# Kernel optimization log

Measured on AMD Instinct MI355X. Metric: run time of the kernel, lower is better.

The kernel has to match this reference:

```python
import jax, jax.numpy as jnp
from jax import lax
import numpy as np

B, T, F = 2048, 256, 64
HIDDEN = [64, 32, 16]
OUT = 1


def _lstm_params(key, in_dim, h):
    k1, k2, k3 = jax.random.split(key, 3)
    s_in = 1.0 / np.sqrt(in_dim)
    s_h = 1.0 / np.sqrt(h)
    W = jax.random.uniform(k1, (in_dim, 4 * h), jnp.float32, -s_in, s_in)
    U = jax.random.uniform(k2, (h, 4 * h), jnp.float32, -s_h, s_h)
    # Keras unit_forget_bias: bias starts at 0 except forget gate = 1
    b = jnp.concatenate([jnp.zeros((h,)), jnp.ones((h,)), jnp.zeros((2 * h,))]).astype(jnp.float32)
    return W, U, b


def setup_inputs() -> dict:
    key = jax.random.key(0)
    ks = jax.random.split(key, 6)
    x = jax.random.normal(ks[0], (B, T, F), jnp.float32)
    W0, U0, b0 = _lstm_params(ks[1], F, HIDDEN[0])
    W1, U1, b1 = _lstm_params(ks[2], HIDDEN[0], HIDDEN[1])
    W2, U2, b2 = _lstm_params(ks[3], HIDDEN[1], HIDDEN[2])
    s = 1.0 / np.sqrt(HIDDEN[2])
    Wd = jax.random.uniform(ks[4], (HIDDEN[2], OUT), jnp.float32, -s, s)
    bd = jnp.zeros((OUT,), jnp.float32)
    return {"x": x, "W0": W0, "U0": U0, "b0": b0,
            "W1": W1, "U1": U1, "b1": b1,
            "W2": W2, "U2": U2, "b2": b2,
            "Wd": Wd, "bd": bd}


def _lstm(x, W, U, b):
    """Keras-style LSTM scan. x: [B,T,in]. Returns (seq [B,T,H], last_h [B,H]).
    Gate order i,f,g,o; recurrent_activation=sigmoid, activation=tanh.
    Dropout/recurrent_dropout are identity at inference (training=False)."""
    Bsz = x.shape[0]
    H = U.shape[0]
    # precompute input projection for all timesteps (one big GEMM)
    xz = jnp.einsum('bti,ig->btg', x, W) + b  # [B,T,4H]
    xz_t = jnp.swapaxes(xz, 0, 1)  # [T,B,4H]

    def step(carry, z_in):
        h, c = carry
        z = z_in + h @ U  # [B,4H]
        i, f, g, o = jnp.split(z, 4, axis=-1)
        i = jax.nn.sigmoid(i)
        f = jax.nn.sigmoid(f)
        g = jnp.tanh(g)
        o = jax.nn.sigmoid(o)
        c = f * c + i * g
        h = o * jnp.tanh(c)
        return (h, c), h

    init = (jnp.zeros((Bsz, H), x.dtype), jnp.zeros((Bsz, H), x.dtype))
    (h_last, _), hs = lax.scan(step, init, xz_t)
    return jnp.swapaxes(hs, 0, 1), h_last


def reference(x, W0, U0, b0, W1, U1, b1, W2, U2, b2, Wd, bd):
    h, _ = _lstm(x, W0, U0, b0)          # return_sequences=True -> [B,T,64]
    h, _ = _lstm(h, W1, U1, b1)          # return_sequences=True -> [B,T,32]
    _, h_last = _lstm(h, W2, U2, b2)     # return_sequences=False -> [B,16]
    return h_last @ Wd + bd              # Dense -> [B,1]
```

## Files before the change

kernel.cpp:

```cpp
#include <hip/hip_runtime.h>


typedef __attribute__((ext_vector_type(8))) short s8v;
typedef __attribute__((ext_vector_type(4))) float f4v;
typedef __attribute__((ext_vector_type(2))) unsigned uint2v;
typedef unsigned short ushort_t;

#define T_STEPS 256
#define BT 8

#define XH  0
#define XL  2048
#define H0H 4096
#define H0L 6144
#define H1H 8192
#define H1L 9216
#define H2H 10240
#define H2L 11264
#define SM_SHORTS 12288

#define PIN(v) asm volatile("" : "+v"(v))
#define BAR()  asm volatile("s_waitcnt lgkmcnt(0)\n\ts_barrier" ::: "memory")

__device__ __forceinline__ unsigned short f2bf(float f) {
    unsigned u = __float_as_uint(f);
    u += 0x7fff + ((u >> 16) & 1);
    return (unsigned short)(u >> 16);
}
__device__ __forceinline__ float bf2f(unsigned short s) {
    return __uint_as_float(((unsigned)s) << 16);
}
__device__ __forceinline__ void tsplit(float v, unsigned short& hi, unsigned short& lo) {
    unsigned u = __float_as_uint(v);
    hi = (unsigned short)(u >> 16);
    float r = v - __uint_as_float(u & 0xffff0000u);
    lo = (unsigned short)(__float_as_uint(r) >> 16);
}
__device__ __forceinline__ float sigmoid_f(float x) {
    return __builtin_amdgcn_rcpf(1.0f + __expf(-x));
}
__device__ __forceinline__ float tanh_f(float x) {
    return 1.0f - 2.0f * __builtin_amdgcn_rcpf(__expf(2.0f * x) + 1.0f);
}

__device__ __forceinline__ float sel_swap(float a, float b) {
    uint2v r = __builtin_amdgcn_permlane32_swap(__float_as_uint(a), __float_as_uint(b), false, false);
    return __uint_as_float(r[0]);
}

__device__ __forceinline__ float wval(const float* W, const float* U,
                                      int inDim, int KH, int fourH, int k, int n) {
    if (k < inDim) return W[k * fourH + n];
    if (k < KH)    return U[(k - inDim) * fourH + n];
    return 0.0f;
}
__device__ __forceinline__ void load_bfrag(const float* W, const float* U,
                                           int inDim, int KH, int fourH,
                                           int k0, int n, s8v& hi, s8v& lo) {
#pragma unroll
    for (int j = 0; j < 8; ++j) {
        float w = wval(W, U, inDim, KH, fourH, k0 + j, n);
        unsigned short h = f2bf(w);
        unsigned short l = f2bf(w - bf2f(h));
        hi[j] = (short)h;
        lo[j] = (short)l;
    }
}

__device__ __forceinline__ void gates2(const f4v* acc, float* c, float* hn) {
#pragma unroll
    for (int j = 0; j < 2; ++j) {
        float zi = sel_swap(acc[0][j], acc[0][j + 2]);
        float zf = sel_swap(acc[1][j], acc[1][j + 2]);
        float zg = sel_swap(acc[2][j], acc[2][j + 2]);
        float zo = sel_swap(acc[3][j], acc[3][j + 2]);
        float ig = sigmoid_f(zi);
        float fg = sigmoid_f(zf);
        float gg = tanh_f(zg);
        float og = sigmoid_f(zo);
        c[j] = fmaf(fg, c[j], ig * gg);
        hn[j] = og * tanh_f(c[j]);
    }
}

__global__ __attribute__((amdgpu_flat_work_group_size(512, 512),
                          amdgpu_waves_per_eu(2, 2)))
void lstm_pipe(const float* __restrict__ x,
               const float* __restrict__ W0, const float* __restrict__ U0, const float* __restrict__ b0,
               const float* __restrict__ W1, const float* __restrict__ U1, const float* __restrict__ b1,
               const float* __restrict__ W2, const float* __restrict__ U2, const float* __restrict__ b2,
               const float* __restrict__ Wd, const float* __restrict__ bd,
               float* __restrict__ out)
{
    const int tid  = threadIdx.x;
    const int lane = tid & 63;
    const int wv   = tid >> 6;
    const int fr   = lane >> 4;
    const int fc   = lane & 15;
    const int bbase = blockIdx.x * BT;

    __shared__ __align__(16) ushort_t SMEM[SM_SHORTS];
    __shared__ __align__(16) float h2last[BT][16];

    {
        unsigned* p32 = (unsigned*)SMEM;
        for (int i = tid; i < SM_SHORTS / 2; i += 512) p32[i] = 0u;
    }
    __syncthreads();

    const ushort_t* rb = SMEM + lane * 8;
    const int rowb = (fr & 1) * 4 + ((fr >> 1) << 1);

    if (wv < 4) {
        s8v Bh[4][4], Bl[4][4];
        float bias[4];
#pragma unroll
        for (int g = 0; g < 4; ++g) {
            int n = g * 64 + wv * 16 + fc;
            bias[g] = b0[n];
#pragma unroll
            for (int kc = 0; kc < 4; ++kc)
                load_bfrag(W0, U0, 64, 128, 256, kc * 32 + fr * 8, n, Bh[g][kc], Bl[g][kc]);
        }
#pragma unroll
        for (int g = 0; g < 4; ++g) {
            PIN(bias[g]);
#pragma unroll
            for (int kc = 0; kc < 4; ++kc) { PIN(Bh[g][kc]); PIN(Bl[g][kc]); }
        }
        float c0[2] = {0.f, 0.f};
        const int hq  = wv >> 1;
        const int k   = (wv & 1) * 16 + fc;
        const int ibw = (k >> 3) * 128 + (k & 7);
        __syncthreads();
        for (int s = 0; s < T_STEPS + 2; ++s) {
            if (s < T_STEPS) {
                const ushort_t* r = rb + ((s & 1) << 10);
                s8v ah[4], al[4];
                ah[0] = *(const s8v*)&r[XH  +   0];
                al[0] = *(const s8v*)&r[XL  +   0];
                ah[1] = *(const s8v*)&r[XH  + 512];
                al[1] = *(const s8v*)&r[XL  + 512];
                ah[2] = *(const s8v*)&r[H0H +   0];
                al[2] = *(const s8v*)&r[H0L +   0];
                ah[3] = *(const s8v*)&r[H0H + 512];
                al[3] = *(const s8v*)&r[H0L + 512];
                f4v acc[4];
#pragma unroll
                for (int g = 0; g < 4; ++g) acc[g] = (f4v){bias[g], bias[g], bias[g], bias[g]};
#pragma unroll
                for (int kc = 0; kc < 4; ++kc) {
#pragma unroll
                    for (int g = 0; g < 4; ++g)
                        acc[g] = __builtin_amdgcn_mfma_f32_16x16x32_bf16(ah[kc], Bh[g][kc], acc[g], 0, 0, 0);
#pragma unroll
                    for (int g = 0; g < 4; ++g)
                        acc[g] = __builtin_amdgcn_mfma_f32_16x16x32_bf16(al[kc], Bh[g][kc], acc[g], 0, 0, 0);
#pragma unroll
                    for (int g = 0; g < 4; ++g)
                        acc[g] = __builtin_amdgcn_mfma_f32_16x16x32_bf16(ah[kc], Bl[g][kc], acc[g], 0, 0, 0);
                }
                float hn[2];
                gates2(acc, c0, hn);
                {
                    ushort_t* w = SMEM + (((s & 1) ^ 1) << 10) + hq * 512 + ibw;
#pragma unroll
                    for (int j = 0; j < 2; ++j) {
                        unsigned short hh_, ll_;
                        tsplit(hn[j], hh_, ll_);
                        w[H0H + (rowb + j) * 8] = hh_;
                        w[H0L + (rowb + j) * 8] = ll_;
                    }
                }
            }
            BAR();
        }
    } else if (wv < 6) {
        s8v Bh[4][3], Bl[4][3];
        float bias[4];
#pragma unroll
        for (int g = 0; g < 4; ++g) {
            int n = g * 32 + (wv & 1) * 16 + fc;
            bias[g] = b1[n];
#pragma unroll
            for (int kc = 0; kc < 3; ++kc)
                load_bfrag(W1, U1, 64, 96, 128, kc * 32 + fr * 8, n, Bh[g][kc], Bl[g][kc]);
        }
#pragma unroll
        for (int g = 0; g < 4; ++g) {
            PIN(bias[g]);
#pragma unroll
            for (int kc = 0; kc < 3; ++kc) { PIN(Bh[g][kc]); PIN(Bl[g][kc]); }
        }
        float c1[2] = {0.f, 0.f};
        const int k   = (wv & 1) * 16 + fc;
        const int ibw = (k >> 3) * 128 + (k & 7);
        __syncthreads();
        for (int s = 0; s < T_STEPS + 2; ++s) {
            if (s >= 1 && s <= T_STEPS) {
                const int p = s & 1;
                const ushort_t* r  = rb + (p << 10);
                const ushort_t* r1 = rb + (p << 9);
                s8v ah[3], al[3];
                ah[0] = *(const s8v*)&r[H0H +   0];
                al[0] = *(const s8v*)&r[H0L +   0];
                ah[1] = *(const s8v*)&r[H0H + 512];
                al[1] = *(const s8v*)&r[H0L + 512];
                ah[2] = *(const s8v*)&r1[H1H];
                al[2] = *(const s8v*)&r1[H1L];
                f4v acc[4];
#pragma unroll
                for (int g = 0; g < 4; ++g) acc[g] = (f4v){bias[g], bias[g], bias[g], bias[g]};
#pragma unroll
                for (int kc = 0; kc < 3; ++kc) {
#pragma unroll
                    for (int g = 0; g < 4; ++g)
                        acc[g] = __builtin_amdgcn_mfma_f32_16x16x32_bf16(ah[kc], Bh[g][kc], acc[g], 0, 0, 0);
#pragma unroll
                    for (int g = 0; g < 4; ++g)
                        acc[g] = __builtin_amdgcn_mfma_f32_16x16x32_bf16(al[kc], Bh[g][kc], acc[g], 0, 0, 0);
#pragma unroll
                    for (int g = 0; g < 4; ++g)
                        acc[g] = __builtin_amdgcn_mfma_f32_16x16x32_bf16(ah[kc], Bl[g][kc], acc[g], 0, 0, 0);
                }
                float hn[2];
                gates2(acc, c1, hn);
                {
                    ushort_t* w = SMEM + ((p ^ 1) << 9) + ibw;
#pragma unroll
                    for (int j = 0; j < 2; ++j) {
                        unsigned short hh_, ll_;
                        tsplit(hn[j], hh_, ll_);
                        w[H1H + (rowb + j) * 8] = hh_;
                        w[H1L + (rowb + j) * 8] = ll_;
                    }
                }
            }
            BAR();
        }
    } else if (wv == 6) {
        s8v Bh[4][2], Bl[4][2];
        float bias[4];
#pragma unroll
        for (int g = 0; g < 4; ++g) {
            int n = g * 16 + fc;
            bias[g] = b2[n];
#pragma unroll
            for (int kc = 0; kc < 2; ++kc)
                load_bfrag(W2, U2, 32, 48, 64, kc * 32 + fr * 8, n, Bh[g][kc], Bl[g][kc]);
        }
#pragma unroll
        for (int g = 0; g < 4; ++g) {
            PIN(bias[g]);
#pragma unroll
            for (int kc = 0; kc < 2; ++kc) { PIN(Bh[g][kc]); PIN(Bl[g][kc]); }
        }
        float c2[2] = {0.f, 0.f};
        const int ibw = (fc >> 3) * 128 + (fc & 7);
        __syncthreads();
        for (int s = 0; s < T_STEPS + 2; ++s) {
            if (s >= 2) {
                const int p = s & 1;
                const ushort_t* r1 = rb + (p << 9);
                s8v ah[2], al[2];
                ah[0] = *(const s8v*)&r1[H1H];
                al[0] = *(const s8v*)&r1[H1L];
                ah[1] = *(const s8v*)&r1[H2H];
                al[1] = *(const s8v*)&r1[H2L];
                f4v acc[4];
#pragma unroll
                for (int g = 0; g < 4; ++g) acc[g] = (f4v){bias[g], bias[g], bias[g], bias[g]};
#pragma unroll
                for (int kc = 0; kc < 2; ++kc) {
#pragma unroll
                    for (int g = 0; g < 4; ++g)
                        acc[g] = __builtin_amdgcn_mfma_f32_16x16x32_bf16(ah[kc], Bh[g][kc], acc[g], 0, 0, 0);
#pragma unroll
                    for (int g = 0; g < 4; ++g)
                        acc[g] = __builtin_amdgcn_mfma_f32_16x16x32_bf16(al[kc], Bh[g][kc], acc[g], 0, 0, 0);
#pragma unroll
                    for (int g = 0; g < 4; ++g)
                        acc[g] = __builtin_amdgcn_mfma_f32_16x16x32_bf16(ah[kc], Bl[g][kc], acc[g], 0, 0, 0);
                }
                float hn[2];
                gates2(acc, c2, hn);
                {
                    ushort_t* w = SMEM + ((p ^ 1) << 9) + ibw;
#pragma unroll
                    for (int j = 0; j < 2; ++j) {
                        unsigned short hh_, ll_;
                        tsplit(hn[j], hh_, ll_);
                        w[H2H + (rowb + j) * 8] = hh_;
                        w[H2L + (rowb + j) * 8] = ll_;
                    }
                    if (s == T_STEPS + 1) {
#pragma unroll
                        for (int j = 0; j < 2; ++j) h2last[rowb + j][fc] = hn[j];
                    }
                }
            }
            BAR();
        }
    } else {
        const int xb = lane >> 3;
        const int fo = (lane & 7) * 8;
        const float* xp = x + ((size_t)(bbase + xb) * T_STEPS) * 64 + fo;
        const int o2 = (fo >> 5) * 512 + (((fo & 31) >> 3) * 16 + xb) * 8;

        auto write_x = [&](float4 v0, float4 v1, int tt) {
            float vv[8] = {v0.x, v0.y, v0.z, v0.w, v1.x, v1.y, v1.z, v1.w};
            s8v hi8, lo8;
#pragma unroll
            for (int j = 0; j < 8; ++j) {
                unsigned short h_, l_;
                tsplit(vv[j], h_, l_);
                hi8[j] = (short)h_;
                lo8[j] = (short)l_;
            }
            ushort_t* wbp = SMEM + ((tt & 1) << 10) + o2;
            *(s8v*)&wbp[XH] = hi8;
            *(s8v*)&wbp[XL] = lo8;
        };

        float4 pa = *(const float4*)(xp);
        float4 pb = *(const float4*)(xp + 4);
        write_x(pa, pb, 0);
        pa = *(const float4*)(xp + 64);
        pb = *(const float4*)(xp + 64 + 4);
        __syncthreads();
        for (int s = 0; s < T_STEPS + 2; ++s) {
            float4 na, nb;
            const bool ld = (s + 2 < T_STEPS);
            if (ld) {
                na = *(const float4*)(xp + (size_t)(s + 2) * 64);
                nb = *(const float4*)(xp + (size_t)(s + 2) * 64 + 4);
            }
            if (s + 1 < T_STEPS) write_x(pa, pb, s + 1);
            if (ld) { pa = na; pb = nb; }
            BAR();
        }
    }

    __syncthreads();
    if (tid < BT) {
        float acc = bd[0];
#pragma unroll
        for (int j = 0; j < 16; ++j) acc += h2last[tid][j] * Wd[j];
        out[bbase + tid] = acc;
    }
}

extern "C" void kernel_launch(void* const* d_in, const int* in_sizes, int n_in,
                              void* d_out, int out_size, void* d_ws, size_t ws_size,
                              hipStream_t stream) {
    (void)in_sizes; (void)n_in; (void)d_ws; (void)ws_size; (void)out_size;
    const float* x  = (const float*)d_in[0];
    const float* W0 = (const float*)d_in[1];
    const float* U0 = (const float*)d_in[2];
    const float* b0 = (const float*)d_in[3];
    const float* W1 = (const float*)d_in[4];
    const float* U1 = (const float*)d_in[5];
    const float* b1 = (const float*)d_in[6];
    const float* W2 = (const float*)d_in[7];
    const float* U2 = (const float*)d_in[8];
    const float* b2 = (const float*)d_in[9];
    const float* Wd = (const float*)d_in[10];
    const float* bd = (const float*)d_in[11];
    float* out = (float*)d_out;

    dim3 grid(2048 / BT);
    dim3 block(512);
    hipLaunchKernelGGL(lstm_pipe, grid, block, 0, stream,
                       x, W0, U0, b0, W1, U1, b1, W2, U2, b2, Wd, bd, out);
}
```

Measured before the change: 414.6 us.

## Batch layer-0 input projection over two timesteps via permlane swap

Layer 0 now computes the input-projection MFMAs for two consecutive timesteps at once: on even steps the x fragment holds two timesteps (packed into separate row halves by the loader warp), and on odd steps the precomputed accumulator half is recovered with a permlane32 swap instead of recomputing. This removes the x-projection MFMAs from every other step on the serial critical path. The loader warp now writes x two steps ahead with a new interleaved LDS layout. The risk is that the packed layout and lane mapping must match exactly, and the extra lookahead adds register pressure.

```diff
diff --git a/kernel.cpp b/kernel.cpp
--- a/kernel.cpp
+++ b/kernel.cpp
@@ -46,6 +46,10 @@
 __device__ __forceinline__ float sel_swap(float a, float b) {
     uint2v r = __builtin_amdgcn_permlane32_swap(__float_as_uint(a), __float_as_uint(b), false, false);
     return __uint_as_float(r[0]);
+}
+__device__ __forceinline__ float swap_hi(float a) {
+    uint2v r = __builtin_amdgcn_permlane32_swap(__float_as_uint(a), __float_as_uint(a), false, false);
+    return __uint_as_float(r[1]);
 }
 
 __device__ __forceinline__ float wval(const float* W, const float* U,
@@ -132,38 +136,70 @@
         const int hq  = wv >> 1;
         const int k   = (wv & 1) * 16 + fc;
         const int ibw = (k >> 3) * 128 + (k & 7);
+        f4v acc[4];
         __syncthreads();
         for (int s = 0; s < T_STEPS + 2; ++s) {
             if (s < T_STEPS) {
-                const ushort_t* r = rb + ((s & 1) << 10);
-                s8v ah[4], al[4];
-                ah[0] = *(const s8v*)&r[XH  +   0];
-                al[0] = *(const s8v*)&r[XL  +   0];
-                ah[1] = *(const s8v*)&r[XH  + 512];
-                al[1] = *(const s8v*)&r[XL  + 512];
-                ah[2] = *(const s8v*)&r[H0H +   0];
-                al[2] = *(const s8v*)&r[H0L +   0];
-                ah[3] = *(const s8v*)&r[H0H + 512];
-                al[3] = *(const s8v*)&r[H0L + 512];
-                f4v acc[4];
-#pragma unroll
-                for (int g = 0; g < 4; ++g) acc[g] = (f4v){bias[g], bias[g], bias[g], bias[g]};
-#pragma unroll
-                for (int kc = 0; kc < 4; ++kc) {
-#pragma unroll
-                    for (int g = 0; g < 4; ++g)
-                        acc[g] = __builtin_amdgcn_mfma_f32_16x16x32_bf16(ah[kc], Bh[g][kc], acc[g], 0, 0, 0);
-#pragma unroll
-                    for (int g = 0; g < 4; ++g)
-                        acc[g] = __builtin_amdgcn_mfma_f32_16x16x32_bf16(al[kc], Bh[g][kc], acc[g], 0, 0, 0);
-#pragma unroll
-                    for (int g = 0; g < 4; ++g)
-                        acc[g] = __builtin_amdgcn_mfma_f32_16x16x32_bf16(ah[kc], Bl[g][kc], acc[g], 0, 0, 0);
-                }
+                const int p = s & 1;
+                const ushort_t* r = rb + (p << 10);
+                s8v hh0 = *(const s8v*)&r[H0H +   0];
+                s8v hl0 = *(const s8v*)&r[H0L +   0];
+                s8v hh1 = *(const s8v*)&r[H0H + 512];
+                s8v hl1 = *(const s8v*)&r[H0L + 512];
+                if (p == 0) {
+                    const ushort_t* rx = rb + (((s >> 1) & 1) << 10);
+                    s8v xh0 = *(const s8v*)&rx[XH +   0];
+                    s8v xl0 = *(const s8v*)&rx[XL +   0];
+                    s8v xh1 = *(const s8v*)&rx[XH + 512];
+                    s8v xl1 = *(const s8v*)&rx[XL + 512];
+#pragma unroll
+                    for (int g = 0; g < 4; ++g) acc[g] = (f4v){bias[g], bias[g], bias[g], bias[g]};
+#pragma unroll
+                    for (int g = 0; g < 4; ++g)
+                        acc[g] = __builtin_amdgcn_mfma_f32_16x16x32_bf16(xh0, Bh[g][0], acc[g], 0, 0, 0);
+#pragma unroll
+                    for (int g = 0; g < 4; ++g)
+                        acc[g] = __builtin_amdgcn_mfma_f32_16x16x32_bf16(xl0, Bh[g][0], acc[g], 0, 0, 0);
+#pragma unroll
+                    for (int g = 0; g < 4; ++g)
+                        acc[g] = __builtin_amdgcn_mfma_f32_16x16x32_bf16(xh0, Bl[g][0], acc[g], 0, 0, 0);
+#pragma unroll
+                    for (int g = 0; g < 4; ++g)
+                        acc[g] = __builtin_amdgcn_mfma_f32_16x16x32_bf16(xh1, Bh[g][1], acc[g], 0, 0, 0);
+#pragma unroll
+                    for (int g = 0; g < 4; ++g)
+                        acc[g] = __builtin_amdgcn_mfma_f32_16x16x32_bf16(xl1, Bh[g][1], acc[g], 0, 0, 0);
+#pragma unroll
+                    for (int g = 0; g < 4; ++g)
+                        acc[g] = __builtin_amdgcn_mfma_f32_16x16x32_bf16(xh1, Bl[g][1], acc[g], 0, 0, 0);
+                } else {
+#pragma unroll
+                    for (int g = 0; g < 4; ++g)
+#pragma unroll
+                        for (int q = 0; q < 4; ++q) acc[g][q] = swap_hi(acc[g][q]);
+                }
+#pragma unroll
+                for (int g = 0; g < 4; ++g)
+                    acc[g] = __builtin_amdgcn_mfma_f32_16x16x32_bf16(hh0, Bh[g][2], acc[g], 0, 0, 0);
+#pragma unroll
+                for (int g = 0; g < 4; ++g)
+                    acc[g] = __builtin_amdgcn_mfma_f32_16x16x32_bf16(hl0, Bh[g][2], acc[g], 0, 0, 0);
+#pragma unroll
+                for (int g = 0; g < 4; ++g)
+                    acc[g] = __builtin_amdgcn_mfma_f32_16x16x32_bf16(hh0, Bl[g][2], acc[g], 0, 0, 0);
+#pragma unroll
+                for (int g = 0; g < 4; ++g)
+                    acc[g] = __builtin_amdgcn_mfma_f32_16x16x32_bf16(hh1, Bh[g][3], acc[g], 0, 0, 0);
+#pragma unroll
+                for (int g = 0; g < 4; ++g)
+                    acc[g] = __builtin_amdgcn_mfma_f32_16x16x32_bf16(hl1, Bh[g][3], acc[g], 0, 0, 0);
+#pragma unroll
+                for (int g = 0; g < 4; ++g)
+                    acc[g] = __builtin_amdgcn_mfma_f32_16x16x32_bf16(hh1, Bl[g][3], acc[g], 0, 0, 0);
                 float hn[2];
                 gates2(acc, c0, hn);
                 {
-                    ushort_t* w = SMEM + (((s & 1) ^ 1) << 10) + hq * 512 + ibw;
+                    ushort_t* w = SMEM + ((p ^ 1) << 10) + hq * 512 + ibw;
 #pragma unroll
                     for (int j = 0; j < 2; ++j) {
                         unsigned short hh_, ll_;
@@ -317,7 +353,7 @@
                 hi8[j] = (short)h_;
                 lo8[j] = (short)l_;
             }
-            ushort_t* wbp = SMEM + ((tt & 1) << 10) + o2;
+            ushort_t* wbp = SMEM + (((tt >> 1) & 1) << 10) + ((tt & 1) << 6) + o2;
             *(s8v*)&wbp[XH] = hi8;
             *(s8v*)&wbp[XL] = lo8;
         };
@@ -327,15 +363,18 @@
         write_x(pa, pb, 0);
         pa = *(const float4*)(xp + 64);
         pb = *(const float4*)(xp + 64 + 4);
+        write_x(pa, pb, 1);
+        pa = *(const float4*)(xp + 128);
+        pb = *(const float4*)(xp + 128 + 4);
         __syncthreads();
         for (int s = 0; s < T_STEPS + 2; ++s) {
             float4 na, nb;
-            const bool ld = (s + 2 < T_STEPS);
+            const bool ld = (s + 3 < T_STEPS);
             if (ld) {
-                na = *(const float4*)(xp + (size_t)(s + 2) * 64);
-                nb = *(const float4*)(xp + (size_t)(s + 2) * 64 + 4);
+                na = *(const float4*)(xp + (size_t)(s + 3) * 64);
+                nb = *(const float4*)(xp + (size_t)(s + 3) * 64 + 4);
             }
-            if (s + 1 < T_STEPS) write_x(pa, pb, s + 1);
+            if (s + 2 < T_STEPS) write_x(pa, pb, s + 2);
             if (ld) { pa = na; pb = nb; }
             BAR();
         }
```

After: 406.9 us. About the same (-1.8%).

## Split each LSTM step into MFMA and gate phases with two barriers per step

Applied to the files above, without the earlier changes.

Each timestep is split into two barrier-separated phases. Layer 0 does its MFMAs, then its gates. Layers 1 and 2 run their gate math for the previous step first and then issue MFMAs, so layers skew and overlap their gate and matrix work differently. Pipeline depth grows by one step. The intent is to shorten the critical path per step by overlapping transcendental gate work with other waves' MFMAs, at the cost of twice as many barriers per step.

```diff
diff --git a/kernel.cpp b/kernel.cpp
--- a/kernel.cpp
+++ b/kernel.cpp
@@ -110,6 +110,7 @@
 
     const ushort_t* rb = SMEM + lane * 8;
     const int rowb = (fr & 1) * 4 + ((fr >> 1) << 1);
+    const int NS = T_STEPS + 3;
 
     if (wv < 4) {
         s8v Bh[4][4], Bl[4][4];
@@ -133,9 +134,12 @@
         const int k   = (wv & 1) * 16 + fc;
         const int ibw = (k >> 3) * 128 + (k & 7);
         __syncthreads();
-        for (int s = 0; s < T_STEPS + 2; ++s) {
-            if (s < T_STEPS) {
-                const ushort_t* r = rb + ((s & 1) << 10);
+        for (int s = 0; s < NS; ++s) {
+            const int p = s & 1;
+            f4v acc[4];
+            const bool on = (s < T_STEPS);
+            if (on) {
+                const ushort_t* r = rb + (p << 10);
                 s8v ah[4], al[4];
                 ah[0] = *(const s8v*)&r[XH  +   0];
                 al[0] = *(const s8v*)&r[XL  +   0];
@@ -145,7 +149,6 @@
                 al[2] = *(const s8v*)&r[H0L +   0];
                 ah[3] = *(const s8v*)&r[H0H + 512];
                 al[3] = *(const s8v*)&r[H0L + 512];
-                f4v acc[4];
 #pragma unroll
                 for (int g = 0; g < 4; ++g) acc[g] = (f4v){bias[g], bias[g], bias[g], bias[g]};
 #pragma unroll
@@ -160,17 +163,18 @@
                     for (int g = 0; g < 4; ++g)
                         acc[g] = __builtin_amdgcn_mfma_f32_16x16x32_bf16(ah[kc], Bl[g][kc], acc[g], 0, 0, 0);
                 }
+            }
+            BAR();
+            if (on) {
                 float hn[2];
                 gates2(acc, c0, hn);
-                {
-                    ushort_t* w = SMEM + (((s & 1) ^ 1) << 10) + hq * 512 + ibw;
-#pragma unroll
-                    for (int j = 0; j < 2; ++j) {
-                        unsigned short hh_, ll_;
-                        tsplit(hn[j], hh_, ll_);
-                        w[H0H + (rowb + j) * 8] = hh_;
-                        w[H0L + (rowb + j) * 8] = ll_;
-                    }
+                ushort_t* w = SMEM + ((p ^ 1) << 10) + hq * 512 + ibw;
+#pragma unroll
+                for (int j = 0; j < 2; ++j) {
+                    unsigned short hh_, ll_;
+                    tsplit(hn[j], hh_, ll_);
+                    w[H0H + (rowb + j) * 8] = hh_;
+                    w[H0L + (rowb + j) * 8] = ll_;
                 }
             }
             BAR();
@@ -195,10 +199,24 @@
         float c1[2] = {0.f, 0.f};
         const int k   = (wv & 1) * 16 + fc;
         const int ibw = (k >> 3) * 128 + (k & 7);
+        f4v acc[4];
         __syncthreads();
-        for (int s = 0; s < T_STEPS + 2; ++s) {
+        for (int s = 0; s < NS; ++s) {
+            const int p = s & 1;
+            if (s >= 2 && s <= T_STEPS + 1) {
+                float hn[2];
+                gates2(acc, c1, hn);
+                ushort_t* w = SMEM + (p << 9) + ibw;
+#pragma unroll
+                for (int j = 0; j < 2; ++j) {
+                    unsigned short hh_, ll_;
+                    tsplit(hn[j], hh_, ll_);
+                    w[H1H + (rowb + j) * 8] = hh_;
+                    w[H1L + (rowb + j) * 8] = ll_;
+                }
+            }
+            BAR();
             if (s >= 1 && s <= T_STEPS) {
-                const int p = s & 1;
                 const ushort_t* r  = rb + (p << 10);
                 const ushort_t* r1 = rb + (p << 9);
                 s8v ah[3], al[3];
@@ -208,7 +226,6 @@
                 al[1] = *(const s8v*)&r[H0L + 512];
                 ah[2] = *(const s8v*)&r1[H1H];
                 al[2] = *(const s8v*)&r1[H1L];
-                f4v acc[4];
 #pragma unroll
                 for (int g = 0; g < 4; ++g) acc[g] = (f4v){bias[g], bias[g], bias[g], bias[g]};
 #pragma unroll
@@ -222,18 +239,6 @@
 #pragma unroll
                     for (int g = 0; g < 4; ++g)
                         acc[g] = __builtin_amdgcn_mfma_f32_16x16x32_bf16(ah[kc], Bl[g][kc], acc[g], 0, 0, 0);
-                }
-                float hn[2];
-                gates2(acc, c1, hn);
-                {
-                    ushort_t* w = SMEM + ((p ^ 1) << 9) + ibw;
-#pragma unroll
-                    for (int j = 0; j < 2; ++j) {
-                        unsigned short hh_, ll_;
-                        tsplit(hn[j], hh_, ll_);
-                        w[H1H + (rowb + j) * 8] = hh_;
-                        w[H1L + (rowb + j) * 8] = ll_;
-                    }
                 }
             }
             BAR();
@@ -257,17 +262,35 @@
         }
         float c2[2] = {0.f, 0.f};
         const int ibw = (fc >> 3) * 128 + (fc & 7);
+        f4v acc[4];
         __syncthreads();
-        for (int s = 0; s < T_STEPS + 2; ++s) {
-            if (s >= 2) {
-                const int p = s & 1;
+        for (int s = 0; s < NS; ++s) {
+            const int p = s & 1;
+            if (s >= 3) {
+                float hn[2];
+                gates2(acc, c2, hn);
+                ushort_t* w = SMEM + ((p ^ 1) << 9) + ibw;
+#pragma unroll
+                for (int j = 0; j < 2; ++j) {
+                    unsigned short hh_, ll_;
+                    tsplit(hn[j], hh_, ll_);
+                    w[H2H + (rowb + j) * 8] = hh_;
+                    w[H2L + (rowb + j) * 8] = ll_;
+                }
+                if (s == T_STEPS + 2) {
+#pragma unroll
+                    for (int j = 0; j < 2; ++j) h2last[rowb + j][fc] = hn[j];
+                }
+            }
+            BAR();
+            if (s >= 2 && s <= T_STEPS + 1) {
                 const ushort_t* r1 = rb + (p << 9);
+                const ushort_t* r2 = rb + ((p ^ 1) << 9);
                 s8v ah[2], al[2];
                 ah[0] = *(const s8v*)&r1[H1H];
                 al[0] = *(const s8v*)&r1[H1L];
-                ah[1] = *(const s8v*)&r1[H2H];
-                al[1] = *(const s8v*)&r1[H2L];
-                f4v acc[4];
+                ah[1] = *(const s8v*)&r2[H2H];
+                al[1] = *(const s8v*)&r2[H2L];
 #pragma unroll
                 for (int g = 0; g < 4; ++g) acc[g] = (f4v){bias[g], bias[g], bias[g], bias[g]};
 #pragma unroll
@@ -281,22 +304,6 @@
 #pragma unroll
                     for (int g = 0; g < 4; ++g)
                         acc[g] = __builtin_amdgcn_mfma_f32_16x16x32_bf16(ah[kc], Bl[g][kc], acc[g], 0, 0, 0);
-                }
-                float hn[2];
-                gates2(acc, c2, hn);
-                {
-                    ushort_t* w = SMEM + ((p ^ 1) << 9) + ibw;
-#pragma unroll
-                    for (int j = 0; j < 2; ++j) {
-                        unsigned short hh_, ll_;
-                        tsplit(hn[j], hh_, ll_);
-                        w[H2H + (rowb + j) * 8] = hh_;
-                        w[H2L + (rowb + j) * 8] = ll_;
-                    }
-                    if (s == T_STEPS + 1) {
-#pragma unroll
-                        for (int j = 0; j < 2; ++j) h2last[rowb + j][fc] = hn[j];
-                    }
                 }
             }
             BAR();
@@ -328,13 +335,14 @@
         pa = *(const float4*)(xp + 64);
         pb = *(const float4*)(xp + 64 + 4);
         __syncthreads();
-        for (int s = 0; s < T_STEPS + 2; ++s) {
+        for (int s = 0; s < NS; ++s) {
             float4 na, nb;
             const bool ld = (s + 2 < T_STEPS);
             if (ld) {
                 na = *(const float4*)(xp + (size_t)(s + 2) * 64);
                 nb = *(const float4*)(xp + (size_t)(s + 2) * 64 + 4);
             }
+            BAR();
             if (s + 1 < T_STEPS) write_x(pa, pb, s + 1);
             if (ld) { pa = na; pb = nb; }
             BAR();
```

Result: slower. 427.0 us (+3.0%).
